# Kernel optimization log

Hardware: AMD Instinct MI355X
Metric: run time of the kernel (lower is better)

## Reference

```python
import jax, jax.numpy as jnp
import numpy as np

K = 40        # knn neighbors (hard-coded in forward)
BN_EPS = 1e-5
NEG_SLOPE = 0.2
NHEADS = 8
ADIM = 64
HDIM = NHEADS * ADIM  # 512
SCALE = HDIM ** (-0.5)  # note: original scales by hdim**-0.5, not adim**-0.5


def knn_idx(x, k):
    # x: (B, C, N) -> (B, N, k) indices of k nearest neighbors (incl. self)
    xx = jnp.sum(x * x, axis=1)                       # (B, N)
    inner = jnp.einsum('bcn,bcm->bnm', x, x)          # (B, N, N)
    neg_sq_dist = 2.0 * inner - xx[:, :, None] - xx[:, None, :]
    return jax.lax.top_k(neg_sq_dist, k)[1]           # (B, N, k)


def get_graph_feature(x, k):
    # x: (B, C, N) -> (B, 2C, N, k)
    idx = knn_idx(x, k)                               # (B, N, k) int32
    xt = jnp.transpose(x, (0, 2, 1))                  # (B, N, C)
    feat = jax.vmap(lambda pts, ids: pts[ids])(xt, idx)  # (B, N, k, C)
    center = xt[:, :, None, :]                        # (B, N, 1, C)
    out = jnp.concatenate(
        [feat - center, jnp.broadcast_to(center, feat.shape)], axis=-1)
    return jnp.transpose(out, (0, 3, 1, 2))           # (B, 2C, N, k)


def bn_lrelu(h, g, b, m, v):
    # inference-mode BatchNorm2d over channel axis=1 + LeakyReLU(0.2)
    scale = g / jnp.sqrt(v + BN_EPS)
    h = (h - m[None, :, None, None]) * scale[None, :, None, None] + b[None, :, None, None]
    return jax.nn.leaky_relu(h, NEG_SLOPE)


def branch(p, conv5_w, bn5_g, bn5_b, bn5_m, bn5_v, conv6_w, bn6_g, bn6_b, bn6_m, bn6_v):
    g = get_graph_feature(p, K)                       # (B, 1024, N, k)
    h = jnp.einsum('oc,bcnk->bonk', conv5_w, g)       # (B, 512, N, k)
    h = bn_lrelu(h, bn5_g, bn5_b, bn5_m, bn5_v)
    h = jnp.transpose(h, (0, 2, 1, 3))                # (B, N=2048, 512, k)
    h = jnp.einsum('oc,bcnk->bonk', conv6_w, h)       # (B, 515, 512, k)
    h = bn_lrelu(h, bn6_g, bn6_b, bn6_m, bn6_v)
    h = jnp.transpose(h, (0, 2, 1, 3))                # (B, 512, 515, k)
    return jnp.max(h, axis=-1)                        # (B, 512, 515)


def heads(f, W):
    # f: (B, S, indim), W: (hdim, indim) -> (B, nheads, S, adim)
    q = jnp.einsum('bsi,oi->bso', f, W)
    B, S, _ = q.shape
    return jnp.transpose(q.reshape(B, S, NHEADS, ADIM), (0, 2, 1, 3))


def setup_inputs() -> dict:
    key = jax.random.key(0)
    ks = jax.random.split(key, 8)
    B, C, N = 1, 512, 2048
    indim = 515
    inp = {
        'x': jax.random.normal(ks[0], (B, C, N), jnp.float32),
        'y': jax.random.normal(ks[1], (B, C, N), jnp.float32),
        'conv5_w': jax.random.normal(ks[2], (512, 1024), jnp.float32) * 0.02,
        'bn5_g': jnp.ones((512,), jnp.float32),
        'bn5_b': jnp.zeros((512,), jnp.float32),
        'bn5_m': jnp.zeros((512,), jnp.float32),
        'bn5_v': jnp.ones((512,), jnp.float32),
        'conv6_w': jax.random.normal(ks[3], (515, 2048), jnp.float32) * 0.02,
        'bn6_g': jnp.ones((515,), jnp.float32),
        'bn6_b': jnp.zeros((515,), jnp.float32),
        'bn6_m': jnp.zeros((515,), jnp.float32),
        'bn6_v': jnp.ones((515,), jnp.float32),
        'Wq': jax.random.normal(ks[4], (HDIM, indim), jnp.float32) * 0.02,
        'Wk': jax.random.normal(ks[5], (HDIM, indim), jnp.float32) * 0.02,
        'Wv': jax.random.normal(ks[6], (HDIM, indim), jnp.float32) * 0.02,
        'Wout': jax.random.normal(ks[7], (indim, HDIM), jnp.float32) * 0.02,
        'bout': jnp.zeros((indim,), jnp.float32),
    }
    return inp


def reference(x, y, conv5_w, bn5_g, bn5_b, bn5_m, bn5_v,
              conv6_w, bn6_g, bn6_b, bn6_m, bn6_v,
              Wq, Wk, Wv, Wout, bout):
    xf = branch(x, conv5_w, bn5_g, bn5_b, bn5_m, bn5_v,
                conv6_w, bn6_g, bn6_b, bn6_m, bn6_v)   # (B, 512, 515)
    yf = branch(y, conv5_w, bn5_g, bn5_b, bn5_m, bn5_v,
                conv6_w, bn6_g, bn6_b, bn6_m, bn6_v)   # (B, 512, 515)
    q = heads(xf, Wq)                                  # (B, H, 512, adim)
    k = heads(yf, Wk)
    v = heads(yf, Wv)
    scores = jax.nn.softmax(jnp.einsum('bhsd,bhtd->bhst', q, k) * SCALE, axis=-1)
    weighted = jnp.einsum('bhst,bhtd->bhsd', scores, v)  # (B, H, 512, adim)
    B, H, S, D = weighted.shape
    merged = jnp.transpose(weighted, (0, 2, 1, 3)).reshape(B, S, H * D)
    return jnp.einsum('bsh,oh->bso', merged, Wout) + bout  # (B, 512, 515)
```

## Files before the change

### kernel.cpp

```cpp
#include <hip/hip_runtime.h>
#include <hip/hip_bf16.h>

typedef __bf16 bf16_t;
typedef float f32x4 __attribute__((ext_vector_type(4)));
typedef __bf16 bf16x8 __attribute__((ext_vector_type(8)));

#define ASYNC_COPY16(gptr, lptr) \
    __builtin_amdgcn_global_load_lds((const __attribute__((address_space(1))) void*)(gptr), \
                                     (__attribute__((address_space(3))) void*)(lptr), 16, 0, 0)

__device__ __forceinline__ float ldx(const void* p, long i, int isbf) {
    return isbf ? (float)((const bf16_t*)p)[i] : ((const float*)p)[i];
}

__global__ __launch_bounds__(256)
void detect_dtype(const void* __restrict__ x, int n, int* __restrict__ flags)
{
    __shared__ int red[4];
    const int tid = threadIdx.x;
    const int ns = n < 8192 ? n : 8192;
    int cnt = 0;
    for (int i = tid; i < ns; i += 256) {
        float v = (float)((const bf16_t*)x)[i];
        float a = fabsf(v);
        bool pl = (v == 0.f) || (a >= 6e-8f && a <= 1.7e7f);
        cnt += pl ? 1 : 0;
    }
    for (int o = 32; o; o >>= 1) cnt += __shfl_down(cnt, o);
    if ((tid & 63) == 0) red[tid >> 6] = cnt;
    __syncthreads();
    if (tid == 0) {
        int t = red[0] + red[1] + red[2] + red[3];
        flags[0] = (t * 10 >= ns * 9) ? 1 : 0;
    }
}

__global__ __launch_bounds__(256)
void conv_elem(const void* __restrict__ src, bf16_t* __restrict__ dst, int n,
               const int* __restrict__ flag)
{
    const int isbf = *flag;
    for (long i = blockIdx.x * 256L + threadIdx.x; i < n; i += (long)gridDim.x * 256)
        dst[i] = (bf16_t)ldx(src, i, isbf);
}

struct P9 { const void* p[9]; int n[9]; };
__global__ __launch_bounds__(256)
void conv_param(P9 pk, float* __restrict__ dst, const int* __restrict__ flag)
{
    const int isbf = *flag;
    const int b = blockIdx.x, n = pk.n[b];
    for (int j = threadIdx.x; j < n; j += 256)
        dst[b * 544 + j] = ldx(pk.p[b], j, isbf);
}

__global__ __launch_bounds__(256)
void pad_wf(const void* __restrict__ W, bf16_t* __restrict__ Wp, const int* __restrict__ flag)
{
    const int isbf = *flag;
    const long i = blockIdx.x * 256L + threadIdx.x;
    if (i >= 512 * 544) return;
    const long o = i / 544, c = i % 544;
    Wp[i] = (c < 515) ? (bf16_t)ldx(W, o * 515 + c, isbf) : (bf16_t)0.f;
}

__global__ __launch_bounds__(256)
void transpose_split(const void* __restrict__ X, bf16_t* __restrict__ XtA,
                     bf16_t* __restrict__ XtB, const int* __restrict__ flag)
{
    __shared__ __align__(16) bf16_t thi[32][33];
    __shared__ __align__(16) bf16_t tlo[32][33];
    const int isbf = *flag;
    const int n0 = blockIdx.x * 32, c0 = blockIdx.y * 32;
    const int lx = threadIdx.x & 31, ly = threadIdx.x >> 5;
    for (int i = 0; i < 4; ++i) {
        float v = ldx(X, (long)(c0 + ly + i * 8) * 2048 + n0 + lx, isbf);
        bf16_t hi = (bf16_t)v;
        thi[ly + i * 8][lx] = hi;
        tlo[ly + i * 8][lx] = (bf16_t)(v - (float)hi);
    }
    __syncthreads();
    for (int i = 0; i < 4; ++i) {
        const long n = n0 + ly + i * 8;
        const int c = c0 + lx;
        bf16_t hi = thi[lx][ly + i * 8], lo = tlo[lx][ly + i * 8];
        XtA[n * 1536 + c] = hi;  XtA[n * 1536 + 512 + c] = lo;  XtA[n * 1536 + 1024 + c] = hi;
        XtB[n * 1536 + c] = hi;  XtB[n * 1536 + 512 + c] = hi;  XtB[n * 1536 + 1024 + c] = lo;
    }
}

__global__ __launch_bounds__(256)
void xx_kernel(const bf16_t* __restrict__ XtA, float* __restrict__ xx)
{
    const long n = blockIdx.x * 256L + threadIdx.x;
    float acc = 0.f;
    for (int c = 0; c < 512; ++c) {
        float v = (float)XtA[n * 1536 + c] + (float)XtA[n * 1536 + 512 + c];
        acc += v * v;
    }
    xx[n] = acc;
}

__global__ __launch_bounds__(256)
void gemm128d(const bf16_t* __restrict__ A, const bf16_t* __restrict__ B,
              float* __restrict__ C, int M, int N, int K, int lda, int ldb, int ldc)
{
    __shared__ __align__(16) bf16_t As[2][4096];
    __shared__ __align__(16) bf16_t Bs[2][4096];
    const int tid = threadIdx.x;
    int mt, nt;
    if ((gridDim.y & 7) == 0) {
        const int bid = blockIdx.y * gridDim.x + blockIdx.x;
        const int xcd = bid & 7, s = bid >> 3;
        mt = s % gridDim.x;
        nt = xcd + 8 * (s / gridDim.x);
    } else { mt = blockIdx.x; nt = blockIdx.y; }
    const int m0 = mt * 128, n0 = nt * 128;
    const int wave = tid >> 6, lane = tid & 63;
    const int wm = (wave >> 1) * 64, wn = (wave & 1) * 64;
    const int l15 = lane & 15, quad = lane >> 4;

    const bf16_t* ga[2]; const bf16_t* gb[2]; int loff[2];
    for (int i = 0; i < 2; ++i) {
        const int q = wave * 2 + i;
        const int seg = q & 3, half = q >> 2;
        const int row = half * 64 + lane;
        long ar = min((long)(m0 + row), (long)M - 1);
        long br = min((long)(n0 + row), (long)N - 1);
        ga[i] = A + ar * lda + seg * 8;
        gb[i] = B + br * ldb + seg * 8;
        loff[i] = seg * 1024 + half * 512;
    }

    f32x4 acc[4][4] = {};

    for (int i = 0; i < 2; ++i) {
        ASYNC_COPY16(ga[i], &As[0][loff[i]]);
        ASYNC_COPY16(gb[i], &Bs[0][loff[i]]);
    }

    for (int k0 = 0; k0 < K; k0 += 32) {
        const int cur = (k0 >> 5) & 1;
        __syncthreads();
        if (k0 + 32 < K) {
            for (int i = 0; i < 2; ++i) {
                ASYNC_COPY16(ga[i] + k0 + 32, &As[cur ^ 1][loff[i]]);
                ASYNC_COPY16(gb[i] + k0 + 32, &Bs[cur ^ 1][loff[i]]);
            }
        }
        bf16x8 af[4], bfr[4];
        for (int mi = 0; mi < 4; ++mi)
            af[mi] = *(const bf16x8*)&As[cur][quad * 1024 + (wm + mi * 16 + l15) * 8];
        for (int ni = 0; ni < 4; ++ni)
            bfr[ni] = *(const bf16x8*)&Bs[cur][quad * 1024 + (wn + ni * 16 + l15) * 8];
        for (int mi = 0; mi < 4; ++mi)
        for (int ni = 0; ni < 4; ++ni)
            acc[mi][ni] = __builtin_amdgcn_mfma_f32_16x16x32_bf16(af[mi], bfr[ni], acc[mi][ni], 0, 0, 0);
    }

    for (int mi = 0; mi < 4; ++mi)
    for (int ni = 0; ni < 4; ++ni)
    for (int r = 0; r < 4; ++r) {
        int gm = m0 + wm + mi * 16 + quad * 4 + r;
        int gn = n0 + wn + ni * 16 + l15;
        if (gm >= M || gn >= N) continue;
        C[(long)gm * ldc + gn] = acc[mi][ni][r];
    }
}

__global__ __launch_bounds__(256)
void epi6_max(const float* __restrict__ C2c, const float* __restrict__ p6,
              bf16_t* __restrict__ Fb, int c0, int Nc)
{
    const int cl = blockIdx.x, tid = threadIdx.x;
    for (int o2 = tid; o2 < 544; o2 += 256) {
        float r = 0.f;
        if (o2 < 515) {
            const float sc = p6[o2] / sqrtf(p6[3 * 544 + o2] + 1e-5f);
            const float mu = p6[2 * 544 + o2], bb = p6[1 * 544 + o2];
            const float* p = C2c + (long)o2 * Nc + cl * 40;
            float mx = -__builtin_inff();
            for (int k = 0; k < 40; ++k) {
                float h = (p[k] - mu) * sc + bb;
                h = h >= 0.f ? h : 0.2f * h;
                mx = fmaxf(mx, h);
            }
            r = mx;
        }
        Fb[(long)(c0 + cl) * 544 + o2] = (bf16_t)r;
    }
}

__global__ __launch_bounds__(256)
void gemm64d(const bf16_t* __restrict__ A, const bf16_t* __restrict__ B,
             float* __restrict__ C, const float* __restrict__ xx,
             int M, int N, int K, int lda, int ldb, int ldc,
             long aBS, long bBS, long cBS, int epi, int moff)
{
    __shared__ __align__(16) bf16_t As[2][4 * 64 * 8];
    __shared__ __align__(16) bf16_t Bs[2][4 * 64 * 8];
    const int tid = threadIdx.x;
    const int m0 = blockIdx.y * 64, n0 = blockIdx.x * 64;
    const int bz = blockIdx.z;
    A += (long)bz * aBS;
    B += (long)bz * bBS;
    const int wave = tid >> 6, lane = tid & 63;
    const int wm = (wave >> 1) * 32, wn = (wave & 1) * 32;
    const int l15 = lane & 15, quad = lane >> 4;

    const long ar = min((long)(m0 + lane), (long)M - 1);
    const long br = min((long)(n0 + lane), (long)N - 1);
    const bf16_t* ga = A + ar * lda + wave * 8;
    const bf16_t* gb = B + br * ldb + wave * 8;

    f32x4 acc[2][2] = {};

    ASYNC_COPY16(ga, &As[0][wave * 512]);
    ASYNC_COPY16(gb, &Bs[0][wave * 512]);

    for (int k0 = 0; k0 < K; k0 += 32) {
        const int cur = (k0 >> 5) & 1;
        __syncthreads();
        if (k0 + 32 < K) {
            ASYNC_COPY16(ga + k0 + 32, &As[cur ^ 1][wave * 512]);
            ASYNC_COPY16(gb + k0 + 32, &Bs[cur ^ 1][wave * 512]);
        }
        bf16x8 af0 = *(const bf16x8*)&As[cur][quad * 512 + (wm +      l15) * 8];
        bf16x8 af1 = *(const bf16x8*)&As[cur][quad * 512 + (wm + 16 + l15) * 8];
        bf16x8 bf0 = *(const bf16x8*)&Bs[cur][quad * 512 + (wn +      l15) * 8];
        bf16x8 bf1 = *(const bf16x8*)&Bs[cur][quad * 512 + (wn + 16 + l15) * 8];
        acc[0][0] = __builtin_amdgcn_mfma_f32_16x16x32_bf16(af0, bf0, acc[0][0], 0, 0, 0);
        acc[0][1] = __builtin_amdgcn_mfma_f32_16x16x32_bf16(af0, bf1, acc[0][1], 0, 0, 0);
        acc[1][0] = __builtin_amdgcn_mfma_f32_16x16x32_bf16(af1, bf0, acc[1][0], 0, 0, 0);
        acc[1][1] = __builtin_amdgcn_mfma_f32_16x16x32_bf16(af1, bf1, acc[1][1], 0, 0, 0);
    }

    C += (long)bz * cBS;
    for (int mi = 0; mi < 2; ++mi)
    for (int ni = 0; ni < 2; ++ni)
    for (int r = 0; r < 4; ++r) {
        int gm = m0 + wm + mi * 16 + quad * 4 + r;
        int gn = n0 + wn + ni * 16 + l15;
        if (gm >= M || gn >= N) continue;
        float o = acc[mi][ni][r];
        long cidx = (long)gm * ldc + gn;
        if (epi == 1) C[cidx] = 2.f * o - xx[gm + moff] - xx[gn];
        else          C[cidx] = o;
    }
}

__global__ __launch_bounds__(256)
void gemm_nt(const bf16_t* __restrict__ A, const bf16_t* __restrict__ B,
             void* __restrict__ Cv, const float* __restrict__ bias,
             const int* __restrict__ oflag, float alpha,
             int M, int N, int K, int lda, int ldb, int ldc,
             long aBS, long bBS, long cBS, int epi)
{
    __shared__ __align__(16) bf16_t As[64 * 40];
    __shared__ __align__(16) bf16_t Bs[64 * 40];
    const int tid = threadIdx.x;
    const int m0 = blockIdx.y * 64, n0 = blockIdx.x * 64;
    const int bz = blockIdx.z;
    A += (long)bz * aBS;
    B += (long)bz * bBS;

    const int lrow = tid >> 2;
    const int lseg = (tid & 3) * 8;
    const long arow = min(m0 + lrow, M - 1);
    const long brow = min(n0 + lrow, N - 1);
    const bf16_t* ap = A + arow * lda + lseg;
    const bf16_t* bp = B + brow * ldb + lseg;

    const int wave = tid >> 6, lane = tid & 63;
    const int wm = (wave >> 1) * 32, wn = (wave & 1) * 32;
    const int l15 = lane & 15, quad = lane >> 4;

    f32x4 acc[2][2] = {};

    for (int k0 = 0; k0 < K; k0 += 32) {
        int4 av = *(const int4*)ap;  ap += 32;
        int4 bv = *(const int4*)bp;  bp += 32;
        __syncthreads();
        *(int4*)(&As[lrow * 40 + lseg]) = av;
        *(int4*)(&Bs[lrow * 40 + lseg]) = bv;
        __syncthreads();
        bf16x8 af0 = *(const bf16x8*)(&As[(wm +      l15) * 40 + quad * 8]);
        bf16x8 af1 = *(const bf16x8*)(&As[(wm + 16 + l15) * 40 + quad * 8]);
        bf16x8 bf0 = *(const bf16x8*)(&Bs[(wn +      l15) * 40 + quad * 8]);
        bf16x8 bf1 = *(const bf16x8*)(&Bs[(wn + 16 + l15) * 40 + quad * 8]);
        acc[0][0] = __builtin_amdgcn_mfma_f32_16x16x32_bf16(af0, bf0, acc[0][0], 0, 0, 0);
        acc[0][1] = __builtin_amdgcn_mfma_f32_16x16x32_bf16(af0, bf1, acc[0][1], 0, 0, 0);
        acc[1][0] = __builtin_amdgcn_mfma_f32_16x16x32_bf16(af1, bf0, acc[1][0], 0, 0, 0);
        acc[1][1] = __builtin_amdgcn_mfma_f32_16x16x32_bf16(af1, bf1, acc[1][1], 0, 0, 0);
    }

    const int ofl = oflag ? *oflag : 1;
    for (int mi = 0; mi < 2; ++mi)
    for (int ni = 0; ni < 2; ++ni)
    for (int r = 0; r < 4; ++r) {
        int gm = m0 + wm + mi * 16 + quad * 4 + r;
        int gn = n0 + wn + ni * 16 + l15;
        if (gm >= M || gn >= N) continue;
        float o = acc[mi][ni][r];
        long cidx = (long)bz * cBS + (long)gm * ldc + gn;
        switch (epi) {
        case 2: ((bf16_t*)Cv)[cidx] = (bf16_t)o; break;
        case 3: ((float*)Cv)[cidx] = o * alpha; break;
        case 5: ((bf16_t*)Cv)[(long)bz * cBS + (long)gn * ldc + gm] = (bf16_t)o; break;
        case 6: {
            float w = o + bias[gn];
            if (ofl) ((bf16_t*)Cv)[cidx] = (bf16_t)w;
            else     ((float*)Cv)[cidx]  = w;
        } break;
        }
    }
}

__global__ __launch_bounds__(256)
void topk40_bs(const float* __restrict__ S, int* __restrict__ idx_out)
{
    __shared__ int red[4];
    __shared__ unsigned long long tmask[8][4];
    __shared__ int sh_slot;
    __shared__ unsigned cu[48];
    __shared__ int      ci[48];
    const int row = blockIdx.x, tid = threadIdx.x;
    const int wave = tid >> 6, lane = tid & 63;

    unsigned uvr[8];
    for (int c = 0; c < 8; ++c) {
        unsigned x = __float_as_uint(S[(long)row * 2048 + c * 256 + tid]);
        uvr[c] = (x & 0x80000000u) ? ~x : (x | 0x80000000u);
    }
    if (tid == 0) sh_slot = 0;

    unsigned lo = 0u, hi = 0xFFFFFFFFu;
    while (hi - lo > 1u) {
        unsigned mid = lo + ((hi - lo) >> 1);
        int c = 0;
        for (int i = 0; i < 8; ++i) c += (uvr[i] > mid) ? 1 : 0;
        for (int o = 32; o; o >>= 1) c += __shfl_down(c, o);
        if (lane == 0) red[wave] = c;
        __syncthreads();
        int tot = red[0] + red[1] + red[2] + red[3];
        __syncthreads();
        if (tot >= 40) lo = mid; else hi = mid;
    }
    const unsigned thr = hi;

    for (int c = 0; c < 8; ++c)
        if (uvr[c] > thr) {
            int s = atomicAdd(&sh_slot, 1);
            cu[s] = uvr[c]; ci[s] = c * 256 + tid;
        }
    for (int c = 0; c < 8; ++c) {
        unsigned long long m = __ballot(uvr[c] == thr);
        if (lane == 0) tmask[c][wave] = m;
    }
    __syncthreads();
    const int want = 40 - sh_slot;
    int base = 0;
    for (int c = 0; c < 8; ++c) {
        if (uvr[c] == thr) {
            int r = base;
            for (int w = 0; w < wave; ++w) r += __popcll(tmask[c][w]);
            r += __popcll(tmask[c][wave] & (((unsigned long long)1 << lane) - 1));
            if (r < want) {
                int s = atomicAdd(&sh_slot, 1);
                cu[s] = uvr[c]; ci[s] = c * 256 + tid;
            }
        }
        for (int w = 0; w < 4; ++w) base += __popcll(tmask[c][w]);
    }
    __syncthreads();
    if (tid < 40) {
        unsigned u = cu[tid]; int i = ci[tid];
        int r = 0;
        for (int j = 0; j < 40; ++j)
            r += (cu[j] > u || (cu[j] == u && ci[j] < i)) ? 1 : 0;
        idx_out[row * 40 + r] = i;
    }
}

__global__ __launch_bounds__(256)
void h1a_gen(const float* __restrict__ T, const float* __restrict__ U,
             const int* __restrict__ idx, const float* __restrict__ pf,
             bf16_t* __restrict__ Hc, int c0)
{
    __shared__ int idxs[40 * 256];
    const int c5 = c0 + blockIdx.y, n0 = blockIdx.x * 256, tid = threadIdx.x;
    for (int i = tid; i < 40 * 256; i += 256)
        idxs[(i % 40) * 256 + (i / 40)] = idx[n0 * 40 + i] & 2047;
    const float sc = pf[c5] / sqrtf(pf[3 * 544 + c5] + 1e-5f);
    const float mu = pf[2 * 544 + c5], bb = pf[1 * 544 + c5];
    const float q  = U[(long)c5 * 2048 + n0 + tid] - T[(long)c5 * 2048 + n0 + tid];
    const float* Trow = T + (long)c5 * 2048;
    __syncthreads();
    for (int k = 0; k < 40; ++k) {
        float h = Trow[idxs[k * 256 + tid]] + q;
        h = (h - mu) * sc + bb;
        h = h >= 0.f ? h : 0.2f * h;
        Hc[(long)(blockIdx.y * 40 + k) * 2048 + n0 + tid] = (bf16_t)h;
    }
}

__global__ __launch_bounds__(256)
void softmax_row(const float* __restrict__ Sc, bf16_t* __restrict__ P)
{
    __shared__ float red[4];
    const long r = blockIdx.x;
    const int tid = threadIdx.x, lane = tid & 63, wave = tid >> 6;
    const float* row = Sc + r * 512;
    float v0 = row[tid], v1 = row[tid + 256];
    float mx = fmaxf(v0, v1);
    for (int off = 32; off; off >>= 1) mx = fmaxf(mx, __shfl_down(mx, off));
    if (lane == 0) red[wave] = mx;
    __syncthreads();
    mx = fmaxf(fmaxf(red[0], red[1]), fmaxf(red[2], red[3]));
    __syncthreads();
    float e0 = expf(v0 - mx), e1 = expf(v1 - mx);
    float sm = e0 + e1;
    for (int off = 32; off; off >>= 1) sm += __shfl_down(sm, off);
    if (lane == 0) red[wave] = sm;
    __syncthreads();
    sm = red[0] + red[1] + red[2] + red[3];
    float inv = 1.f / sm;
    P[r * 512 + tid] = (bf16_t)(e0 * inv);
    P[r * 512 + tid + 256] = (bf16_t)(e1 * inv);
}

extern "C" void kernel_launch(void* const* d_in, const int* in_sizes, int n_in,
                              void* d_out, int out_size, void* d_ws, size_t ws_size,
                              hipStream_t stream)
{
    (void)n_in; (void)out_size;

    char* wsb = (char*)d_ws;
    size_t pos = 0;
    auto alloc = [&](size_t bytes) -> char* {
        char* p = wsb + pos;
        pos += (bytes + 255) & ~(size_t)255;
        return p;
    };
    int*    flags = (int*)  alloc(256);
    int*    idx   = (int*)  alloc(2048 * 40 * 4);
    float*  xx    = (float*)alloc(2048 * 4);
    float*  T     = (float*)alloc((size_t)512 * 2048 * 4);
    float*  U     = (float*)alloc((size_t)512 * 2048 * 4);
    bf16_t* XtA   = (bf16_t*)alloc((size_t)2048 * 1536 * 2);
    bf16_t* XtB   = (bf16_t*)alloc((size_t)2048 * 1536 * 2);
    bf16_t* W5c   = (bf16_t*)alloc((size_t)512 * 1024 * 2);
    bf16_t* W6c   = (bf16_t*)alloc((size_t)515 * 2048 * 2);
    bf16_t* Woutc = (bf16_t*)alloc((size_t)515 * 512 * 2);
    bf16_t* Wqp   = (bf16_t*)alloc((size_t)512 * 544 * 2);
    bf16_t* Wkp   = (bf16_t*)alloc((size_t)512 * 544 * 2);
    bf16_t* Wvp   = (bf16_t*)alloc((size_t)512 * 544 * 2);
    float*  pf    = (float*)alloc((size_t)9 * 544 * 4);
    bf16_t* Fb[2];
    Fb[0] = (bf16_t*)alloc((size_t)512 * 544 * 2);
    Fb[1] = (bf16_t*)alloc((size_t)512 * 544 * 2);
    bf16_t* qb = (bf16_t*)alloc((size_t)512 * 512 * 2);
    bf16_t* kb = (bf16_t*)alloc((size_t)512 * 512 * 2);
    bf16_t* vt = (bf16_t*)alloc((size_t)512 * 512 * 2);
    bf16_t* mg = (bf16_t*)alloc((size_t)512 * 512 * 2);
    char* BIG = wsb + pos;
    size_t big = (ws_size > pos) ? (ws_size - pos) : 0;
    if (big < 3939840) return;

    const int CC = (big >= 126074880) ? 512 : (big >= 63037440) ? 256
                 : (big >= 31518720)  ? 128 : (big >= 15759360) ? 64
                 : (big >= 7879680)   ? 32  : 16;
    const int RC = (big >= 16777216) ? 2048 : (big >= 4194304) ? 512 : 128;
    const int AH = (big >= 12582912) ? 8 : 1;
    const int Nc = CC * 40;

    float*  S   = (float*)BIG;
    bf16_t* Hc  = (bf16_t*)BIG;
    float*  C2c = (float*)(BIG + (size_t)Nc * 2048 * 2);
    float*  scA = (float*)BIG;
    bf16_t* prA = (bf16_t*)(BIG + (size_t)AH * 512 * 512 * 4);

    detect_dtype<<<1, 256, 0, stream>>>(d_in[0], in_sizes[0], flags);
    conv_elem<<<1024, 256, 0, stream>>>(d_in[2], W5c, 512 * 1024, flags);
    conv_elem<<<1024, 256, 0, stream>>>(d_in[7], W6c, 515 * 2048, flags);
    conv_elem<<<1024, 256, 0, stream>>>(d_in[15], Woutc, 515 * 512, flags);
    pad_wf<<<1088, 256, 0, stream>>>(d_in[12], Wqp, flags);
    pad_wf<<<1088, 256, 0, stream>>>(d_in[13], Wkp, flags);
    pad_wf<<<1088, 256, 0, stream>>>(d_in[14], Wvp, flags);
    P9 pk;
    const int pidx[9] = {3, 4, 5, 6, 8, 9, 10, 11, 16};
    for (int i = 0; i < 9; ++i) { pk.p[i] = d_in[pidx[i]]; pk.n[i] = in_sizes[pidx[i]]; }
    conv_param<<<9, 256, 0, stream>>>(pk, pf, flags);

    for (int b = 0; b < 2; ++b) {
        transpose_split<<<dim3(64, 16), 256, 0, stream>>>(d_in[b], XtA, XtB, flags);
        xx_kernel<<<8, 256, 0, stream>>>(XtA, xx);
        for (int r0 = 0; r0 < 2048; r0 += RC) {
            gemm64d<<<dim3(32, RC / 64), 256, 0, stream>>>(XtA + (size_t)r0 * 1536, XtB, S,
                xx, RC, 2048, 1536, 1536, 1536, 2048, 0, 0, 0, 1, r0);
            topk40_bs<<<RC, 256, 0, stream>>>(S, idx + (size_t)r0 * 40);
        }
        gemm64d<<<dim3(32, 8, 2), 256, 0, stream>>>(W5c, XtA, T, nullptr,
            512, 2048, 512, 1024, 1536, 2048, 512, 0, (long)512 * 2048, 0, 0);
        for (int c0 = 0; c0 < 512; c0 += CC) {
            h1a_gen<<<dim3(8, CC), 256, 0, stream>>>(T, U, idx, pf, Hc, c0);
            gemm128d<<<dim3(5, Nc / 128), 256, 0, stream>>>(W6c, Hc, C2c,
                515, Nc, 2048, 2048, 2048, Nc);
            epi6_max<<<CC, 256, 0, stream>>>(C2c, pf + 4 * 544, Fb[b], c0, Nc);
        }
    }

    gemm_nt<<<dim3(8, 8, 1), 256, 0, stream>>>(Fb[0], Wqp, qb, nullptr, nullptr, 0.f,
        512, 512, 544, 544, 544, 512, 0, 0, 0, 2);
    gemm_nt<<<dim3(8, 8, 1), 256, 0, stream>>>(Fb[1], Wkp, kb, nullptr, nullptr, 0.f,
        512, 512, 544, 544, 544, 512, 0, 0, 0, 2);
    gemm_nt<<<dim3(8, 8, 1), 256, 0, stream>>>(Fb[1], Wvp, vt, nullptr, nullptr, 0.f,
        512, 512, 544, 544, 544, 512, 0, 0, 0, 5);

    const float SCALE = 0.04419417382415922f;
    if (AH == 8) {
        gemm_nt<<<dim3(8, 8, 8), 256, 0, stream>>>(qb, kb, scA, nullptr, nullptr, SCALE,
            512, 512, 64, 512, 512, 512, 64, 64, 262144, 3);
        softmax_row<<<4096, 256, 0, stream>>>(scA, prA);
        gemm_nt<<<dim3(1, 8, 8), 256, 0, stream>>>(prA, vt, mg, nullptr, nullptr, 0.f,
            512, 64, 512, 512, 512, 512, 262144, 32768, 64, 2);
    } else {
        for (int h = 0; h < 8; ++h) {
            gemm_nt<<<dim3(8, 8, 1), 256, 0, stream>>>(qb + h * 64, kb + h * 64, scA,
                nullptr, nullptr, SCALE, 512, 512, 64, 512, 512, 512, 0, 0, 0, 3);
            softmax_row<<<512, 256, 0, stream>>>(scA, prA);
            gemm_nt<<<dim3(1, 8, 1), 256, 0, stream>>>(prA, vt + (size_t)h * 64 * 512,
                mg + h * 64, nullptr, nullptr, 0.f,
                512, 64, 512, 512, 512, 512, 0, 0, 0, 2);
        }
    }
    gemm_nt<<<dim3(9, 8, 1), 256, 0, stream>>>(mg, Woutc, d_out, pf + 8 * 544, flags,
        0.f, 512, 515, 512, 512, 512, 515, 0, 0, 0, 6);
}
```

Measured before the change: 909.3 us.

## Exploit kNN distance symmetry, batch weight-conversion launches, vectorize max epilogue

New measurement: 875.3 us. 1.04x faster.

```diff
diff --git a/kernel.cpp b/kernel.cpp
--- a/kernel.cpp
+++ b/kernel.cpp
@@ -35,11 +35,14 @@
     }
 }
 
-__global__ __launch_bounds__(256)
-void conv_elem(const void* __restrict__ src, bf16_t* __restrict__ dst, int n,
-               const int* __restrict__ flag)
+struct C3 { const void* p[3]; bf16_t* d[3]; int n[3]; };
+__global__ __launch_bounds__(256)
+void conv_elem3(C3 c, const int* __restrict__ flag)
 {
     const int isbf = *flag;
+    const int z = blockIdx.z, n = c.n[z];
+    bf16_t* dst = c.d[z];
+    const void* src = c.p[z];
     for (long i = blockIdx.x * 256L + threadIdx.x; i < n; i += (long)gridDim.x * 256)
         dst[i] = (bf16_t)ldx(src, i, isbf);
 }
@@ -54,14 +57,17 @@
         dst[b * 544 + j] = ldx(pk.p[b], j, isbf);
 }
 
-__global__ __launch_bounds__(256)
-void pad_wf(const void* __restrict__ W, bf16_t* __restrict__ Wp, const int* __restrict__ flag)
+struct P3 { const void* p[3]; };
+__global__ __launch_bounds__(256)
+void pad_wf3(P3 ps, bf16_t* __restrict__ Wp0, const int* __restrict__ flag)
 {
     const int isbf = *flag;
+    const int z = blockIdx.z;
     const long i = blockIdx.x * 256L + threadIdx.x;
     if (i >= 512 * 544) return;
     const long o = i / 544, c = i % 544;
-    Wp[i] = (c < 515) ? (bf16_t)ldx(W, o * 515 + c, isbf) : (bf16_t)0.f;
+    bf16_t* Wp = Wp0 + (size_t)z * 512 * 544;
+    Wp[i] = (c < 515) ? (bf16_t)ldx(ps.p[z], o * 515 + c, isbf) : (bf16_t)0.f;
 }
 
 __global__ __launch_bounds__(256)
@@ -178,12 +184,16 @@
         if (o2 < 515) {
             const float sc = p6[o2] / sqrtf(p6[3 * 544 + o2] + 1e-5f);
             const float mu = p6[2 * 544 + o2], bb = p6[1 * 544 + o2];
-            const float* p = C2c + (long)o2 * Nc + cl * 40;
+            const float4* p = (const float4*)(C2c + (long)o2 * Nc + cl * 40);
             float mx = -__builtin_inff();
-            for (int k = 0; k < 40; ++k) {
-                float h = (p[k] - mu) * sc + bb;
-                h = h >= 0.f ? h : 0.2f * h;
-                mx = fmaxf(mx, h);
+            for (int k4 = 0; k4 < 10; ++k4) {
+                float4 v = p[k4];
+                float hv[4] = {v.x, v.y, v.z, v.w};
+                for (int j = 0; j < 4; ++j) {
+                    float h = (hv[j] - mu) * sc + bb;
+                    h = h >= 0.f ? h : 0.2f * h;
+                    mx = fmaxf(mx, h);
+                }
             }
             r = mx;
         }
@@ -201,6 +211,7 @@
     __shared__ __align__(16) bf16_t Bs[2][4 * 64 * 8];
     const int tid = threadIdx.x;
     const int m0 = blockIdx.y * 64, n0 = blockIdx.x * 64;
+    if (epi == 4 && n0 < m0) return;
     const int bz = blockIdx.z;
     A += (long)bz * aBS;
     B += (long)bz * bBS;
@@ -243,9 +254,15 @@
         int gn = n0 + wn + ni * 16 + l15;
         if (gm >= M || gn >= N) continue;
         float o = acc[mi][ni][r];
-        long cidx = (long)gm * ldc + gn;
-        if (epi == 1) C[cidx] = 2.f * o - xx[gm + moff] - xx[gn];
-        else          C[cidx] = o;
+        if (epi == 4) {
+            float v = 2.f * o - xx[gm] - xx[gn];
+            C[(long)gm * ldc + gn] = v;
+            C[(long)gn * ldc + gm] = v;
+        } else if (epi == 1) {
+            C[(long)gm * ldc + gn] = 2.f * o - xx[gm + moff] - xx[gn];
+        } else {
+            C[(long)gm * ldc + gn] = o;
+        }
     }
 }
 
@@ -481,12 +498,14 @@
     bf16_t* prA = (bf16_t*)(BIG + (size_t)AH * 512 * 512 * 4);
 
     detect_dtype<<<1, 256, 0, stream>>>(d_in[0], in_sizes[0], flags);
-    conv_elem<<<1024, 256, 0, stream>>>(d_in[2], W5c, 512 * 1024, flags);
-    conv_elem<<<1024, 256, 0, stream>>>(d_in[7], W6c, 515 * 2048, flags);
-    conv_elem<<<1024, 256, 0, stream>>>(d_in[15], Woutc, 515 * 512, flags);
-    pad_wf<<<1088, 256, 0, stream>>>(d_in[12], Wqp, flags);
-    pad_wf<<<1088, 256, 0, stream>>>(d_in[13], Wkp, flags);
-    pad_wf<<<1088, 256, 0, stream>>>(d_in[14], Wvp, flags);
+    C3 c3;
+    c3.p[0] = d_in[2];  c3.d[0] = W5c;   c3.n[0] = 512 * 1024;
+    c3.p[1] = d_in[7];  c3.d[1] = W6c;   c3.n[1] = 515 * 2048;
+    c3.p[2] = d_in[15]; c3.d[2] = Woutc; c3.n[2] = 515 * 512;
+    conv_elem3<<<dim3(512, 1, 3), 256, 0, stream>>>(c3, flags);
+    P3 p3;
+    p3.p[0] = d_in[12]; p3.p[1] = d_in[13]; p3.p[2] = d_in[14];
+    pad_wf3<<<dim3(1088, 1, 3), 256, 0, stream>>>(p3, Wqp, flags);
     P9 pk;
     const int pidx[9] = {3, 4, 5, 6, 8, 9, 10, 11, 16};
     for (int i = 0; i < 9; ++i) { pk.p[i] = d_in[pidx[i]]; pk.n[i] = in_sizes[pidx[i]]; }
@@ -495,10 +514,16 @@
     for (int b = 0; b < 2; ++b) {
         transpose_split<<<dim3(64, 16), 256, 0, stream>>>(d_in[b], XtA, XtB, flags);
         xx_kernel<<<8, 256, 0, stream>>>(XtA, xx);
-        for (int r0 = 0; r0 < 2048; r0 += RC) {
-            gemm64d<<<dim3(32, RC / 64), 256, 0, stream>>>(XtA + (size_t)r0 * 1536, XtB, S,
-                xx, RC, 2048, 1536, 1536, 1536, 2048, 0, 0, 0, 1, r0);
-            topk40_bs<<<RC, 256, 0, stream>>>(S, idx + (size_t)r0 * 40);
+        if (RC == 2048) {
+            gemm64d<<<dim3(32, 32), 256, 0, stream>>>(XtA, XtB, S,
+                xx, 2048, 2048, 1536, 1536, 1536, 2048, 0, 0, 0, 4, 0);
+            topk40_bs<<<2048, 256, 0, stream>>>(S, idx);
+        } else {
+            for (int r0 = 0; r0 < 2048; r0 += RC) {
+                gemm64d<<<dim3(32, RC / 64), 256, 0, stream>>>(XtA + (size_t)r0 * 1536, XtB, S,
+                    xx, RC, 2048, 1536, 1536, 1536, 2048, 0, 0, 0, 1, r0);
+                topk40_bs<<<RC, 256, 0, stream>>>(S, idx + (size_t)r0 * 40);
+            }
         }
         gemm64d<<<dim3(32, 8, 2), 256, 0, stream>>>(W5c, XtA, T, nullptr,
             512, 2048, 512, 1024, 1536, 2048, 512, 0, (long)512 * 2048, 0, 0);
@@ -510,10 +535,9 @@
         }
     }
 
-    gemm_nt<<<dim3(8, 8, 1), 256, 0, stream>>>(Fb[0], Wqp, qb, nullptr, nullptr, 0.f,
-        512, 512, 544, 544, 544, 512, 0, 0, 0, 2);
-    gemm_nt<<<dim3(8, 8, 1), 256, 0, stream>>>(Fb[1], Wkp, kb, nullptr, nullptr, 0.f,
-        512, 512, 544, 544, 544, 512, 0, 0, 0, 2);
+    gemm_nt<<<dim3(8, 8, 2), 256, 0, stream>>>(Fb[0], Wqp, qb, nullptr, nullptr, 0.f,
+        512, 512, 544, 544, 544, 512,
+        (long)512 * 544, (long)512 * 544, (long)512 * 512, 2);
     gemm_nt<<<dim3(8, 8, 1), 256, 0, stream>>>(Fb[1], Wvp, vt, nullptr, nullptr, 0.f,
         512, 512, 544, 544, 544, 512, 0, 0, 0, 5);
 
```
